# Optimization experiments

Hardware: AMD Instinct MI355X
Metric: run time of the kernel (lower is better)

The kernel has to match this reference:

```python
import jax, jax.numpy as jnp
import numpy as np

B, N, H, W = 2, 1024, 128, 128
SH_K = 27  # (sh_degree+1)^2 * 3 for sh_degree=2
L_L1, L_SSIM, L_DEPTH, L_OPAC = 0.8, 0.2, 0.5, 0.01
C0 = 0.28209479177387814


def _quat_to_rot(q):
    # q: [..., 4] (w,x,y,z) -> [..., 3, 3]
    w, x, y, z = q[..., 0], q[..., 1], q[..., 2], q[..., 3]
    R = jnp.stack([1 - 2 * (y * y + z * z), 2 * (x * y - w * z), 2 * (x * z + w * y),
                   2 * (x * y + w * z), 1 - 2 * (x * x + z * z), 2 * (y * z - w * x),
                   2 * (x * z - w * y), 2 * (y * z + w * x), 1 - 2 * (x * x + y * y)], axis=-1)
    return R.reshape(q.shape[:-1] + (3, 3))


def _ssim_window(size=7, sigma=1.5):
    coords = np.arange(size, dtype=np.float32) - size // 2
    g = np.exp(-coords ** 2 / (2 * sigma ** 2))
    g = g / g.sum()
    w2 = np.outer(g, g).astype(np.float32)
    return jnp.asarray(np.broadcast_to(w2[None, None], (3, 1, size, size)))  # OIHW, groups=3


def _dwconv(img, w):
    return jax.lax.conv_general_dilated(img, w, (1, 1), 'SAME',
                                        dimension_numbers=('NCHW', 'OIHW', 'NCHW'),
                                        feature_group_count=3)


def _ssim(img1, img2):
    C1, C2 = 0.01 ** 2, 0.03 ** 2
    w = _ssim_window()
    mu1, mu2 = _dwconv(img1, w), _dwconv(img2, w)
    s1 = _dwconv(img1 * img1, w) - mu1 ** 2
    s2 = _dwconv(img2 * img2, w) - mu2 ** 2
    s12 = _dwconv(img1 * img2, w) - mu1 * mu2
    return jnp.mean((2 * mu1 * mu2 + C1) * (2 * s12 + C2) /
                    ((mu1 ** 2 + mu2 ** 2 + C1) * (s1 + s2 + C2)))


def _render(gaussians, intrinsics):
    means = gaussians[:, :, :3]
    scales = gaussians[:, :, 3:6]
    rots = gaussians[:, :, 6:10]
    opac = gaussians[:, :, 10]        # [B,N]
    sh = gaussians[:, :, 11:]
    fx = intrinsics[:, 0, 0][:, None]
    fy = intrinsics[:, 1, 1][:, None]
    cx = intrinsics[:, 0, 2][:, None]
    cy = intrinsics[:, 1, 2][:, None]
    z = jnp.maximum(means[:, :, 2], 1e-4)
    px = fx * means[:, :, 0] / z + cx
    py = fy * means[:, :, 1] / z + cy
    # ---- 2D covariance (EWA) ----
    R = _quat_to_rot(rots)                               # [B,N,3,3]
    RS = R * scales[:, :, None, :]                        # R @ diag(s)
    cov3d = RS @ jnp.swapaxes(RS, -1, -2)
    zc = jnp.maximum(means[:, :, 2], 1e-6)
    zsq = zc * zc
    J = jnp.zeros(means.shape[:2] + (2, 3), means.dtype)
    J = J.at[:, :, 0, 0].set(fx / zc)
    J = J.at[:, :, 0, 2].set(-fx * means[:, :, 0] / zsq)
    J = J.at[:, :, 1, 1].set(fy / zc)
    J = J.at[:, :, 1, 2].set(-fy * means[:, :, 1] / zsq)
    cov2d = J @ cov3d @ jnp.swapaxes(J, -1, -2) + 0.3 * jnp.eye(2, dtype=means.dtype)
    det = jnp.maximum(cov2d[:, :, 0, 0] * cov2d[:, :, 1, 1] -
                      cov2d[:, :, 0, 1] * cov2d[:, :, 1, 0], 1e-8)
    inv00 = cov2d[:, :, 1, 1] / det
    inv11 = cov2d[:, :, 0, 0] / det
    inv01 = -cov2d[:, :, 0, 1] / det
    colors = jnp.clip(sh[:, :, :3] * C0 + 0.5, 0.0, 1.0)  # [B,N,3]
    # ---- dense per-pixel splatting ----
    gy = jnp.arange(H, dtype=means.dtype)
    gx = jnp.arange(W, dtype=means.dtype)
    dx = gx[None, None, None, :] - px[:, :, None, None]   # [B,N,1,W] -> bcast [B,N,H,W]
    dy = gy[None, None, :, None] - py[:, :, None, None]
    power = -0.5 * (inv00[:, :, None, None] * dx * dx +
                    2.0 * inv01[:, :, None, None] * dx * dy +
                    inv11[:, :, None, None] * dy * dy)
    alpha = jnp.exp(jnp.clip(power, -10.0, 0.0)) * opac[:, :, None, None]
    alpha = jnp.minimum(alpha, 0.99)
    # ---- depth sort + front-to-back compositing ----
    order = jnp.argsort(z, axis=1)
    alpha_s = jnp.take_along_axis(alpha, order[:, :, None, None], axis=1)
    colors_s = jnp.take_along_axis(colors, order[:, :, None], axis=1)
    depth_s = jnp.take_along_axis(z, order, axis=1)
    cp = jnp.cumprod(1.0 - alpha_s, axis=1)
    Tr = jnp.concatenate([jnp.ones_like(alpha_s[:, :1]), cp[:, :-1]], axis=1)
    weights = Tr * alpha_s                               # [B,N,H,W]
    rgb = jnp.clip(jnp.einsum('bnhw,bnc->bchw', weights, colors_s), 0.0, 1.0)
    depth = jnp.sum(weights * depth_s[:, :, None, None], axis=1, keepdims=True)
    return rgb, depth


def setup_inputs() -> dict:
    key = jax.random.key(0)
    k = jax.random.split(key, 8)
    xy = jax.random.normal(k[0], (B, N, 2)) * 1.0
    zc = jax.random.uniform(k[1], (B, N, 1), minval=0.5, maxval=4.0)
    scales = jax.random.uniform(k[2], (B, N, 3), minval=0.01, maxval=0.1)
    q = jax.random.normal(k[3], (B, N, 4))
    q = q / jnp.linalg.norm(q, axis=-1, keepdims=True)
    opac = jax.nn.sigmoid(jax.random.normal(k[4], (B, N, 1)))
    sh = jax.random.normal(k[5], (B, N, SH_K)) * 0.3
    gaussians = jnp.concatenate([xy, zc, scales, q, opac, sh], axis=-1)  # [B,N,38]
    intr = jnp.tile(jnp.array([[120.0, 0.0, 64.0], [0.0, 120.0, 64.0], [0.0, 0.0, 1.0]],
                              dtype=jnp.float32)[None], (B, 1, 1))
    target_rgb = jax.random.uniform(k[6], (B, 3, H, W))
    target_depth = jax.random.uniform(k[7], (B, 1, H, W), minval=0.5, maxval=4.0)
    return {'gaussians': gaussians, 'intrinsics': intr,
            'target_rgb': target_rgb, 'target_depth': target_depth}


def reference(gaussians, intrinsics, target_rgb, target_depth):
    rgb, depth = _render(gaussians, intrinsics)
    l1_rgb = jnp.mean(jnp.abs(rgb - target_rgb))
    ssim_val = _ssim(rgb, target_rgb)
    l1_depth = jnp.mean(jnp.abs(depth - target_depth))
    o = jnp.clip(gaussians[:, :, 10:11], 1e-6, 1.0 - 1e-6)
    opacity_reg = jnp.mean(-(o * jnp.log(o) + (1.0 - o) * jnp.log(1.0 - o)))
    loss = (L_L1 * l1_rgb + L_SSIM * (1.0 - ssim_val) +
            L_DEPTH * l1_depth + L_OPAC * opacity_reg)
    return loss
```

## Files before the change

### kernel.cpp

```cpp
#include <hip/hip_runtime.h>

#define NB 2
#define NG 1024
#define HEIGHT 128
#define WIDTH 128
#define HW (HEIGHT * WIDTH)
#define E10 4.5399931e-05f
#define PW 134
#define PPLANE (PW * PW)

#define REC_S 0
#define P_ENT 32768
#define P_L1D 32800
#define P_SSS 33312
#define P_SSL 33504
#define CNT_I 33696
#define RGBOF 33700

__device__ inline float blk_reduce(float v, float* sh) {
    for (int off = 32; off > 0; off >>= 1) v += __shfl_down(v, off, 64);
    int lane = threadIdx.x & 63;
    int w = threadIdx.x >> 6;
    __syncthreads();
    if (lane == 0) sh[w] = v;
    __syncthreads();
    float s = 0.f;
    if (threadIdx.x == 0) {
        int nw = (blockDim.x + 63) >> 6;
        for (int i = 0; i < nw; i++) s += sh[i];
    }
    return s;
}

__global__ __launch_bounds__(256) void k_prerank(const float* __restrict__ g,
                                                 const float* __restrict__ intr,
                                                 float* __restrict__ ws) {
    __shared__ __align__(16) unsigned long long zkey[NG];
    __shared__ int sp[256];
    int bid = blockIdx.x;
    int b = bid >> 4;
    int grp = bid & 15;
    int tid = threadIdx.x;

#pragma unroll
    for (int q = 0; q < 4; q++) {
        int j = tid + q * 256;
        float z = fmaxf(g[(size_t)((b << 10) + j) * 38 + 2], 1e-4f);
        zkey[j] = ((unsigned long long)__float_as_uint(z) << 10) | (unsigned)j;
    }
    __syncthreads();

    int il = (grp << 6) + (tid & 63);
    int jq = tid >> 6;
    unsigned long long ki = zkey[il];
    int rank = 0;
    int j0 = jq << 8;
#pragma unroll 4
    for (int j = j0; j < j0 + 256; j += 2) {
        ulonglong2 kk = *(const ulonglong2*)(zkey + j);
        rank += (kk.x < ki);
        rank += (kk.y < ki);
    }
    sp[tid] = rank;
    __syncthreads();

    if (tid < 64) {
        int r = sp[tid] + sp[tid + 64] + sp[tid + 128] + sp[tid + 192];
        int idx = (b << 10) + il;
        const float* row = g + (size_t)idx * 38;
        float mx = row[0], my = row[1], mz = row[2];
        float sx = row[3], sy = row[4], sz = row[5];
        float qw = row[6], qx = row[7], qy = row[8], qz = row[9];
        float op = row[10];
        float sh0 = row[11], sh1 = row[12], sh2 = row[13];
        float fx = intr[b * 9 + 0], fy = intr[b * 9 + 4];
        float cx = intr[b * 9 + 2], cy = intr[b * 9 + 5];

        float z = fmaxf(mz, 1e-4f);
        float px = fx * mx / z + cx;
        float py = fy * my / z + cy;

        float r00 = 1.f - 2.f * (qy * qy + qz * qz), r01 = 2.f * (qx * qy - qw * qz), r02 = 2.f * (qx * qz + qw * qy);
        float r10 = 2.f * (qx * qy + qw * qz), r11 = 1.f - 2.f * (qx * qx + qz * qz), r12 = 2.f * (qy * qz - qw * qx);
        float r20 = 2.f * (qx * qz - qw * qy), r21 = 2.f * (qy * qz + qw * qx), r22 = 1.f - 2.f * (qx * qx + qy * qy);
        float a00 = r00 * sx, a01 = r01 * sy, a02 = r02 * sz;
        float a10 = r10 * sx, a11 = r11 * sy, a12 = r12 * sz;
        float a20 = r20 * sx, a21 = r21 * sy, a22 = r22 * sz;
        float m00 = a00 * a00 + a01 * a01 + a02 * a02;
        float m01 = a00 * a10 + a01 * a11 + a02 * a12;
        float m02 = a00 * a20 + a01 * a21 + a02 * a22;
        float m11 = a10 * a10 + a11 * a11 + a12 * a12;
        float m12 = a10 * a20 + a11 * a21 + a12 * a22;
        float m22 = a20 * a20 + a21 * a21 + a22 * a22;

        float zc = fmaxf(mz, 1e-6f);
        float aJ = fx / zc, bJ = -fx * mx / (zc * zc);
        float cJ = fy / zc, dJ = -fy * my / (zc * zc);
        float c00 = aJ * aJ * m00 + 2.f * aJ * bJ * m02 + bJ * bJ * m22 + 0.3f;
        float c01 = cJ * (aJ * m01 + bJ * m12) + dJ * (aJ * m02 + bJ * m22);
        float c11 = cJ * cJ * m11 + 2.f * cJ * dJ * m12 + dJ * dJ * m22 + 0.3f;
        float det = fmaxf(c00 * c11 - c01 * c01, 1e-8f);
        float i00 = c11 / det;
        float i11 = c00 / det;
        float i01 = -c01 / det;

        const float C0c = 0.28209479177387814f;
        float col0 = fminf(fmaxf(sh0 * C0c + 0.5f, 0.f), 1.f);
        float col1 = fminf(fmaxf(sh1 * C0c + 0.5f, 0.f), 1.f);
        float col2 = fminf(fmaxf(sh2 * C0c + 0.5f, 0.f), 1.f);

        float hx = sqrtf(20.f * c00);
        float hy = sqrtf(20.f * c11);

        float* rec = ws + REC_S + (size_t)((b << 10) + r) * 16;
        ((float4*)rec)[0] = make_float4(px, py, hx, hy);
        ((float4*)rec)[1] = make_float4(i00, i01, i11, op);
        ((float4*)rec)[2] = make_float4(col0, col1, col2, z);

        float o = fminf(fmaxf(op, 1e-6f), 1.f - 1e-6f);
        float ent = -(o * logf(o) + (1.f - o) * logf(1.f - o));
        for (int off = 32; off > 0; off >>= 1) ent += __shfl_down(ent, off, 64);
        if (tid == 0) ws[P_ENT + bid] = ent;
    }
    for (int i = bid * 256 + tid; i < 6 * PPLANE; i += 32 * 256)
        ws[RGBOF + i] = 0.f;
    if (bid == 0 && tid == 0) ((int*)ws)[CNT_I] = 0;
}

__global__ __launch_bounds__(1024, 8) void k_render(const float* __restrict__ tgt_d,
                                                    float* __restrict__ ws) {
    __shared__ float4 sPa[NG + 1];
    __shared__ float sPud[NG + 1];
    __shared__ unsigned short slist[NG];
    __shared__ int swcnt[16];
    __shared__ float sagg[16 * 5];
    __shared__ float comb[5][1024];

    int tid = threadIdx.x;
    int lane = tid & 63;
    int wv = tid >> 6;
    int blk = blockIdx.x;
    int b = blk >> 8;
    int tt = blk & 255;
    int x0 = (tt & 15) * 8, y0 = (tt >> 4) * 8;
    int x = x0 + (lane & 7), y = y0 + (lane >> 3);
    float xf = (float)x, yf = (float)y;
    float x0f = (float)x0, x1f = x0f + 7.f;
    float y0f = (float)y0, y1f = y0f + 7.f;

    const float* recs = ws + REC_S + (size_t)(b << 10) * 16;

    const float* rec = recs + (size_t)tid * 16;
    float4 q0 = ((const float4*)rec)[0];
    float4 q1 = ((const float4*)rec)[1];
    float4 q2 = ((const float4*)rec)[2];

    bool ov = (q0.x + q0.z >= x0f) && (q0.x - q0.z <= x1f) &&
              (q0.y + q0.w >= y0f) && (q0.y - q0.w <= y1f);
    unsigned long long mask = __ballot(ov);
    int loff = __popcll(mask & ((1ull << lane) - 1ull));
    if (lane == 0) swcnt[wv] = (int)__popcll(mask);

    float a10 = E10 * q1.w;
    float t = 1.f - a10;
    float ur = a10 * q2.x, ug = a10 * q2.y, ub = a10 * q2.z, ud = a10 * q2.w;
#pragma unroll
    for (int off = 1; off < 64; off <<= 1) {
        float pt = __shfl_up(t, off, 64);
        float pr = __shfl_up(ur, off, 64);
        float pg = __shfl_up(ug, off, 64);
        float pb = __shfl_up(ub, off, 64);
        float pd = __shfl_up(ud, off, 64);
        if (lane >= off) {
            ur = pr + pt * ur; ug = pg + pt * ug;
            ub = pb + pt * ub; ud = pd + pt * ud;
            t = pt * t;
        }
    }
    if (lane == 63) {
        sagg[wv * 5 + 0] = t;  sagg[wv * 5 + 1] = ur; sagg[wv * 5 + 2] = ug;
        sagg[wv * 5 + 3] = ub; sagg[wv * 5 + 4] = ud;
    }
    __syncthreads();

    int woff = 0, cnt = 0;
#pragma unroll
    for (int i = 0; i < 16; i++) {
        int ci = swcnt[i];
        woff += (i < wv) ? ci : 0;
        cnt += ci;
    }
    if (ov) slist[woff + loff] = (unsigned short)tid;

    if (tid < 16) {
        float at = sagg[tid * 5 + 0], ar = sagg[tid * 5 + 1], ag = sagg[tid * 5 + 2];
        float ab = sagg[tid * 5 + 3], ad = sagg[tid * 5 + 4];
#pragma unroll
        for (int off = 1; off < 16; off <<= 1) {
            float pt = __shfl_up(at, off, 16);
            float pr = __shfl_up(ar, off, 16);
            float pg = __shfl_up(ag, off, 16);
            float pb = __shfl_up(ab, off, 16);
            float pd = __shfl_up(ad, off, 16);
            if (tid >= off) {
                ar = pr + pt * ar; ag = pg + pt * ag;
                ab = pb + pt * ab; ad = pd + pt * ad;
                at = pt * at;
            }
        }
        float eat = __shfl_up(at, 1, 16);
        float ear = __shfl_up(ar, 1, 16);
        float eag = __shfl_up(ag, 1, 16);
        float eab = __shfl_up(ab, 1, 16);
        float ead = __shfl_up(ad, 1, 16);
        if (tid == 0) { eat = 1.f; ear = 0.f; eag = 0.f; eab = 0.f; ead = 0.f; }
        sagg[tid * 5 + 0] = eat; sagg[tid * 5 + 1] = ear; sagg[tid * 5 + 2] = eag;
        sagg[tid * 5 + 3] = eab; sagg[tid * 5 + 4] = ead;
    }
    __syncthreads();

    {
        float Pt = sagg[wv * 5 + 0], Pur = sagg[wv * 5 + 1], Pug = sagg[wv * 5 + 2];
        float Pub = sagg[wv * 5 + 3], Pud0 = sagg[wv * 5 + 4];
        sPa[tid + 1] = make_float4(Pt * t, Pur + Pt * ur, Pug + Pt * ug, Pub + Pt * ub);
        sPud[tid + 1] = Pud0 + Pt * ud;
    }
    if (tid == 0) {
        sPa[0] = make_float4(1.f, 0.f, 0.f, 0.f);
        sPud[0] = 0.f;
    }
    __syncthreads();

    int m = (cnt + 15) >> 4;
    int p0 = wv * m; if (p0 > cnt) p0 = cnt;
    int p1 = p0 + m; if (p1 > cnt) p1 = cnt;
    int s0 = (p0 == 0) ? 0 : (int)slist[p0 - 1] + 1;

    float4 Pa = sPa[s0];
    float Pud = sPud[s0];
    float inv0 = 1.f / Pa.x;
    float Pur2 = Pa.y, Pug2 = Pa.z, Pub2 = Pa.w;

    float tau = 1.f, cr = 0.f, cgn = 0.f, cb = 0.f, cd = 0.f;
    int r = (p0 < p1) ? (int)slist[p0] : 0;
    for (int p = p0; p < p1; p++) {
        int rn = (p + 1 < p1) ? (int)slist[p + 1] : 0;
        float4 Qa = sPa[r];
        float Qud = sPud[r];
        const float* rp = recs + (size_t)r * 16;
        float4 g0 = ((const float4*)rp)[0];
        float4 g1 = ((const float4*)rp)[1];
        float4 g2 = ((const float4*)rp)[2];
        float kap = tau * inv0;
        cr += kap * (Qa.y - Pur2);
        cgn += kap * (Qa.z - Pug2);
        cb += kap * (Qa.w - Pub2);
        cd += kap * (Qud - Pud);
        float dx = xf - g0.x, dy = yf - g0.y;
        float q = g1.x * dx * dx + 2.f * g1.y * dx * dy + g1.z * dy * dy;
        float pw = fminf(fmaxf(-0.5f * q, -10.f), 0.f);
        float a = fminf(__expf(pw) * g1.w, 0.99f);
        float w = kap * Qa.x * a;
        cr += w * g2.x; cgn += w * g2.y; cb += w * g2.z; cd += w * g2.w;
        float a10i = E10 * g1.w;
        tau *= (1.f - a) * (1.f + a10i * (1.f + a10i));
        float s = Qa.x * a10i;
        Pur2 = Qa.y + s * g2.x;
        Pug2 = Qa.z + s * g2.y;
        Pub2 = Qa.w + s * g2.z;
        Pud = Qud + s * g2.w;
        r = rn;
    }
    int e0 = (wv == 15) ? NG : ((p1 == 0) ? 0 : (int)slist[p1 - 1] + 1);
    float4 Ea = sPa[e0];
    float Eud = sPud[e0];
    float kapf = tau * inv0;
    cr += kapf * (Ea.y - Pur2);
    cgn += kapf * (Ea.z - Pug2);
    cb += kapf * (Ea.w - Pub2);
    cd += kapf * (Eud - Pud);
    float T = tau * Ea.x * inv0;

    comb[0][tid] = T;
    comb[1][tid] = cr;
    comb[2][tid] = cgn;
    comb[3][tid] = cb;
    comb[4][tid] = cd;
    __syncthreads();

    if (tid < 64) {
        float T0 = comb[0][tid], r0 = comb[1][tid], g0 = comb[2][tid];
        float b0 = comb[3][tid], d0 = comb[4][tid];
#pragma unroll
        for (int sgi = 1; sgi < 16; sgi++) {
            int j = sgi * 64 + tid;
            r0 += T0 * comb[1][j];
            g0 += T0 * comb[2][j];
            b0 += T0 * comb[3][j];
            d0 += T0 * comb[4][j];
            T0 *= comb[0][j];
        }
        r0 = fminf(fmaxf(r0, 0.f), 1.f);
        g0 = fminf(fmaxf(g0, 0.f), 1.f);
        b0 = fminf(fmaxf(b0, 0.f), 1.f);
        float* rgb = ws + RGBOF;
        int pofs = (y + 3) * PW + (x + 3);
        rgb[(b * 3 + 0) * PPLANE + pofs] = r0;
        rgb[(b * 3 + 1) * PPLANE + pofs] = g0;
        rgb[(b * 3 + 2) * PPLANE + pofs] = b0;
        float l1d = fabsf(d0 - tgt_d[(b * HEIGHT + y) * WIDTH + x]);
        for (int off = 32; off > 0; off >>= 1) l1d += __shfl_down(l1d, off, 64);
        if (tid == 0) ws[P_L1D + blk] = l1d;
    }
}

__global__ __launch_bounds__(256) void k_ssim_final(const float* __restrict__ tgt_rgb,
                                                    float* __restrict__ ws,
                                                    float* __restrict__ out) {
    __shared__ float s1[14 * 70];
    __shared__ float s2[14 * 70];
    __shared__ float sh[8];
    __shared__ int sflag;
    int bid = blockIdx.x;
    int tid = threadIdx.x;
    int p = bid >> 5;
    int sy = (bid >> 1) & 15;
    int hx2 = bid & 1;
    int y0 = sy * 8, x0 = hx2 * 64;

    const float* img1p = ws + RGBOF + (size_t)p * PPLANE;
    const float* tgtp = tgt_rgb + (size_t)p * HW;
    for (int i = tid; i < 14 * 70; i += 256) {
        int r = i / 70, c = i - r * 70;
        s1[i] = img1p[(y0 + r) * PW + (x0 + c)];
        int yy = y0 + r - 3, xx = x0 + c - 3;
        float v = 0.f;
        if (yy >= 0 && yy < HEIGHT && xx >= 0 && xx < WIDTH)
            v = tgtp[yy * WIDTH + xx];
        s2[i] = v;
    }
    __syncthreads();

    float gg[7];
    float gs = 0.f;
#pragma unroll
    for (int i = 0; i < 7; i++) {
        float c = (float)(i - 3);
        gg[i] = __expf(-c * c / 4.5f);
        gs += gg[i];
    }
#pragma unroll
    for (int i = 0; i < 7; i++) gg[i] /= gs;

    int row = tid >> 5;
    int colb = (tid & 31) * 2;
    float ssim_acc = 0.f, l1_acc = 0.f;
#pragma unroll
    for (int j = 0; j < 2; j++) {
        int c = colb + j;
        float mu1 = 0.f, mu2 = 0.f, s11 = 0.f, s22 = 0.f, s12 = 0.f;
#pragma unroll
        for (int dy = 0; dy < 7; dy++) {
            int rb = (row + dy) * 70 + c;
#pragma unroll
            for (int dx = 0; dx < 7; dx++) {
                float w = gg[dy] * gg[dx];
                float i1 = s1[rb + dx];
                float i2 = s2[rb + dx];
                mu1 += w * i1;
                mu2 += w * i2;
                s11 += w * i1 * i1;
                s22 += w * i2 * i2;
                s12 += w * i1 * i2;
            }
        }
        float v1 = s11 - mu1 * mu1;
        float v2 = s22 - mu2 * mu2;
        float cv = s12 - mu1 * mu2;
        const float C1 = 1e-4f, C2 = 9e-4f;
        ssim_acc += ((2.f * mu1 * mu2 + C1) * (2.f * cv + C2)) /
                    ((mu1 * mu1 + mu2 * mu2 + C1) * (v1 + v2 + C2));
        int ctr = (row + 3) * 70 + c + 3;
        l1_acc += fabsf(s1[ctr] - s2[ctr]);
    }

    float s_ssim = blk_reduce(ssim_acc, sh);
    float s_l1 = blk_reduce(l1_acc, sh);

    if (tid == 0) {
        ws[P_SSS + bid] = s_ssim;
        ws[P_SSL + bid] = s_l1;
        __threadfence();
        int old = atomicAdd((int*)ws + CNT_I, 1);
        sflag = (old == 191) ? 1 : 0;
    }
    __syncthreads();
    if (sflag) {
        __threadfence();
        float d = 0.f, ss = 0.f, sl = 0.f, e = 0.f;
        for (int i = tid; i < 512; i += 256) d += ws[P_L1D + i];
        if (tid < 192) { ss = ws[P_SSS + tid]; sl = ws[P_SSL + tid]; }
        if (tid < 32) e = ws[P_ENT + tid];
        float rd_ = blk_reduce(d, sh);
        float rss = blk_reduce(ss, sh);
        float rsl = blk_reduce(sl, sh);
        float re = blk_reduce(e, sh);
        if (tid == 0) {
            float l1r = rsl / (float)(NB * 3 * HW);
            float ssimv = rss / (float)(NB * 3 * HW);
            float l1d = rd_ / (float)(NB * HW);
            float opa = re / (float)(NB * NG);
            out[0] = 0.8f * l1r + 0.2f * (1.f - ssimv) + 0.5f * l1d + 0.01f * opa;
        }
    }
}

extern "C" void kernel_launch(void* const* d_in, const int* in_sizes, int n_in,
                              void* d_out, int out_size, void* d_ws, size_t ws_size,
                              hipStream_t stream) {
    const float* g = (const float*)d_in[0];
    const float* intr = (const float*)d_in[1];
    const float* trgb = (const float*)d_in[2];
    const float* tdep = (const float*)d_in[3];
    float* ws = (float*)d_ws;
    float* out = (float*)d_out;

    hipLaunchKernelGGL(k_prerank, dim3(32), dim3(256), 0, stream, g, intr, ws);
    hipLaunchKernelGGL(k_render, dim3(NB * 256), dim3(1024), 0, stream, tdep, ws);
    hipLaunchKernelGGL(k_ssim_final, dim3(192), dim3(256), 0, stream, trgb, ws, out);
}
```

Measured before the change: 92.82 us.

## Hoist per-tile prefix scan into separate per-batch kernel

The per-batch prefix scan of transmittance and colour aggregates was previously recomputed redundantly by each of the 512 render blocks. It now runs once per batch in a new two-block kernel that writes the prefix table to workspace, and the render blocks just load it into shared memory. This removes redundant shuffles and two block barriers per tile. In exchange it adds an extra kernel launch with very low parallelism, plus a global round trip for the table.

After: 94.13 us. About the same (+1.4%).

```diff
diff --git a/kernel.cpp b/kernel.cpp
--- a/kernel.cpp
+++ b/kernel.cpp
@@ -8,6 +8,7 @@
 #define E10 4.5399931e-05f
 #define PW 134
 #define PPLANE (PW * PW)
+#define PFX_STRIDE 8200
 
 #define REC_S 0
 #define P_ENT 32768
@@ -15,7 +16,8 @@
 #define P_SSS 33312
 #define P_SSL 33504
 #define CNT_I 33696
-#define RGBOF 33700
+#define PFX   33700
+#define RGBOF 50100
 
 __device__ inline float blk_reduce(float v, float* sh) {
     for (int off = 32; off > 0; off >>= 1) v += __shfl_down(v, off, 64);
@@ -127,13 +129,80 @@
     if (bid == 0 && tid == 0) ((int*)ws)[CNT_I] = 0;
 }
 
+__global__ __launch_bounds__(1024) void k_scan(float* __restrict__ ws) {
+    __shared__ float sagg[16 * 5];
+    int b = blockIdx.x;
+    int tid = threadIdx.x;
+    int lane = tid & 63;
+    int wv = tid >> 6;
+    const float* rec = ws + REC_S + (size_t)((b << 10) + tid) * 16;
+    float4 q1 = ((const float4*)rec)[1];
+    float4 q2 = ((const float4*)rec)[2];
+    float a10 = E10 * q1.w;
+    float t = 1.f - a10;
+    float ur = a10 * q2.x, ug = a10 * q2.y, ub = a10 * q2.z, ud = a10 * q2.w;
+#pragma unroll
+    for (int off = 1; off < 64; off <<= 1) {
+        float pt = __shfl_up(t, off, 64);
+        float pr = __shfl_up(ur, off, 64);
+        float pg = __shfl_up(ug, off, 64);
+        float pb = __shfl_up(ub, off, 64);
+        float pd = __shfl_up(ud, off, 64);
+        if (lane >= off) {
+            ur = pr + pt * ur; ug = pg + pt * ug;
+            ub = pb + pt * ub; ud = pd + pt * ud;
+            t = pt * t;
+        }
+    }
+    if (lane == 63) {
+        sagg[wv * 5 + 0] = t;  sagg[wv * 5 + 1] = ur; sagg[wv * 5 + 2] = ug;
+        sagg[wv * 5 + 3] = ub; sagg[wv * 5 + 4] = ud;
+    }
+    __syncthreads();
+    if (tid < 16) {
+        float at = sagg[tid * 5 + 0], ar = sagg[tid * 5 + 1], ag = sagg[tid * 5 + 2];
+        float ab = sagg[tid * 5 + 3], ad = sagg[tid * 5 + 4];
+#pragma unroll
+        for (int off = 1; off < 16; off <<= 1) {
+            float pt = __shfl_up(at, off, 16);
+            float pr = __shfl_up(ar, off, 16);
+            float pg = __shfl_up(ag, off, 16);
+            float pb = __shfl_up(ab, off, 16);
+            float pd = __shfl_up(ad, off, 16);
+            if (tid >= off) {
+                ar = pr + pt * ar; ag = pg + pt * ag;
+                ab = pb + pt * ab; ad = pd + pt * ad;
+                at = pt * at;
+            }
+        }
+        float eat = __shfl_up(at, 1, 16);
+        float ear = __shfl_up(ar, 1, 16);
+        float eag = __shfl_up(ag, 1, 16);
+        float eab = __shfl_up(ab, 1, 16);
+        float ead = __shfl_up(ad, 1, 16);
+        if (tid == 0) { eat = 1.f; ear = 0.f; eag = 0.f; eab = 0.f; ead = 0.f; }
+        sagg[tid * 5 + 0] = eat; sagg[tid * 5 + 1] = ear; sagg[tid * 5 + 2] = eag;
+        sagg[tid * 5 + 3] = eab; sagg[tid * 5 + 4] = ead;
+    }
+    __syncthreads();
+    float Pt = sagg[wv * 5 + 0], Pur = sagg[wv * 5 + 1], Pug = sagg[wv * 5 + 2];
+    float Pub = sagg[wv * 5 + 3], Pud = sagg[wv * 5 + 4];
+    float* P = ws + PFX + (size_t)b * PFX_STRIDE;
+    ((float4*)(P + (size_t)(tid + 1) * 8))[0] =
+        make_float4(Pt * t, Pur + Pt * ur, Pug + Pt * ug, Pub + Pt * ub);
+    P[(size_t)(tid + 1) * 8 + 4] = Pud + Pt * ud;
+    if (tid == 0) {
+        ((float4*)P)[0] = make_float4(1.f, 0.f, 0.f, 0.f);
+        P[4] = 0.f;
+    }
+}
+
 __global__ __launch_bounds__(1024, 8) void k_render(const float* __restrict__ tgt_d,
                                                     float* __restrict__ ws) {
     __shared__ float4 sPa[NG + 1];
     __shared__ float sPud[NG + 1];
     __shared__ unsigned short slist[NG];
     __shared__ int swcnt[16];
-    __shared__ float sagg[16 * 5];
     __shared__ float comb[5][1024];
 
     int tid = threadIdx.x;
@@ -150,36 +219,20 @@
 
     const float* recs = ws + REC_S + (size_t)(b << 10) * 16;
 
-    const float* rec = recs + (size_t)tid * 16;
-    float4 q0 = ((const float4*)rec)[0];
-    float4 q1 = ((const float4*)rec)[1];
-    float4 q2 = ((const float4*)rec)[2];
-
+    float4 q0 = ((const float4*)(recs + (size_t)tid * 16))[0];
     bool ov = (q0.x + q0.z >= x0f) && (q0.x - q0.z <= x1f) &&
               (q0.y + q0.w >= y0f) && (q0.y - q0.w <= y1f);
     unsigned long long mask = __ballot(ov);
     int loff = __popcll(mask & ((1ull << lane) - 1ull));
     if (lane == 0) swcnt[wv] = (int)__popcll(mask);
 
-    float a10 = E10 * q1.w;
-    float t = 1.f - a10;
-    float ur = a10 * q2.x, ug = a10 * q2.y, ub = a10 * q2.z, ud = a10 * q2.w;
-#pragma unroll
-    for (int off = 1; off < 64; off <<= 1) {
-        float pt = __shfl_up(t, off, 64);
-        float pr = __shfl_up(ur, off, 64);
-        float pg = __shfl_up(ug, off, 64);
-        float pb = __shfl_up(ub, off, 64);
-        float pd = __shfl_up(ud, off, 64);
-        if (lane >= off) {
-            ur = pr + pt * ur; ug = pg + pt * ug;
-            ub = pb + pt * ub; ud = pd + pt * ud;
-            t = pt * t;
-        }
-    }
-    if (lane == 63) {
-        sagg[wv * 5 + 0] = t;  sagg[wv * 5 + 1] = ur; sagg[wv * 5 + 2] = ug;
-        sagg[wv * 5 + 3] = ub; sagg[wv * 5 + 4] = ud;
+    {
+        const float* P = ws + PFX + (size_t)b * PFX_STRIDE;
+        for (int i = tid; i <= NG; i += 1024) {
+            const float* Pe = P + (size_t)i * 8;
+            sPa[i] = *(const float4*)Pe;
+            sPud[i] = Pe[4];
+        }
     }
     __syncthreads();
 
@@ -191,44 +244,6 @@
         cnt += ci;
     }
     if (ov) slist[woff + loff] = (unsigned short)tid;
-
-    if (tid < 16) {
-        float at = sagg[tid * 5 + 0], ar = sagg[tid * 5 + 1], ag = sagg[tid * 5 + 2];
-        float ab = sagg[tid * 5 + 3], ad = sagg[tid * 5 + 4];
-#pragma unroll
-        for (int off = 1; off < 16; off <<= 1) {
-            float pt = __shfl_up(at, off, 16);
-            float pr = __shfl_up(ar, off, 16);
-            float pg = __shfl_up(ag, off, 16);
-            float pb = __shfl_up(ab, off, 16);
-            float pd = __shfl_up(ad, off, 16);
-            if (tid >= off) {
-                ar = pr + pt * ar; ag = pg + pt * ag;
-                ab = pb + pt * ab; ad = pd + pt * ad;
-                at = pt * at;
-            }
-        }
-        float eat = __shfl_up(at, 1, 16);
-        float ear = __shfl_up(ar, 1, 16);
-        float eag = __shfl_up(ag, 1, 16);
-        float eab = __shfl_up(ab, 1, 16);
-        float ead = __shfl_up(ad, 1, 16);
-        if (tid == 0) { eat = 1.f; ear = 0.f; eag = 0.f; eab = 0.f; ead = 0.f; }
-        sagg[tid * 5 + 0] = eat; sagg[tid * 5 + 1] = ear; sagg[tid * 5 + 2] = eag;
-        sagg[tid * 5 + 3] = eab; sagg[tid * 5 + 4] = ead;
-    }
-    __syncthreads();
-
-    {
-        float Pt = sagg[wv * 5 + 0], Pur = sagg[wv * 5 + 1], Pug = sagg[wv * 5 + 2];
-        float Pub = sagg[wv * 5 + 3], Pud0 = sagg[wv * 5 + 4];
-        sPa[tid + 1] = make_float4(Pt * t, Pur + Pt * ur, Pug + Pt * ug, Pub + Pt * ub);
-        sPud[tid + 1] = Pud0 + Pt * ud;
-    }
-    if (tid == 0) {
-        sPa[0] = make_float4(1.f, 0.f, 0.f, 0.f);
-        sPud[0] = 0.f;
-    }
     __syncthreads();
 
     int m = (cnt + 15) >> 4;
@@ -426,6 +441,7 @@
     float* out = (float*)d_out;
 
     hipLaunchKernelGGL(k_prerank, dim3(32), dim3(256), 0, stream, g, intr, ws);
+    hipLaunchKernelGGL(k_scan, dim3(NB), dim3(1024), 0, stream, ws);
     hipLaunchKernelGGL(k_render, dim3(NB * 256), dim3(1024), 0, stream, tdep, ws);
     hipLaunchKernelGGL(k_ssim_final, dim3(192), dim3(256), 0, stream, trgb, ws, out);
 }
```
